# Kernel tuning notes

Hardware: AMD Instinct MI355X
Metric: run time of the kernel (lower is better)

## Reference

```python
import jax, jax.numpy as jnp
import numpy as np

EPS = 1e-5
SCALE = 4


def _conv(x, w, b=None, stride=1, pad=0):
    y = jax.lax.conv_general_dilated(
        x, w, (stride, stride), ((pad, pad), (pad, pad)),
        dimension_numbers=("NCHW", "OIHW", "NCHW"))
    if b is not None:
        y = y + b[None, :, None, None]
    return y


def _bn(x, g, b, m, v):
    # inference-mode BatchNorm2d with running stats
    scale = g / jnp.sqrt(v + EPS)
    return (x - m[None, :, None, None]) * scale[None, :, None, None] + b[None, :, None, None]


def setup_inputs() -> dict:
    key = jax.random.key(0)
    ks = jax.random.split(key, 20)
    B, H, W = 2, 112, 256
    d = {}
    d["patch"] = jax.random.normal(ks[0], (B, 3, SCALE * H, SCALE * W), jnp.float32)
    d["disp"] = jax.random.normal(ks[1], (B, 1, H, W), jnp.float32)
    # encode: conv(3->256, k=s=4, no bias) + BN + ReLU + conv(256->256, k3 p1, no bias) + BN + ReLU
    d["w_enc1"] = jax.random.normal(ks[2], (256, 3, SCALE, SCALE), jnp.float32) * 0.05
    d["bn1_g"] = jax.random.uniform(ks[3], (256,), jnp.float32) + 0.5
    d["bn1_b"] = jax.random.normal(ks[4], (256,), jnp.float32) * 0.01
    d["bn1_m"] = jax.random.normal(ks[5], (256,), jnp.float32) * 0.01
    d["bn1_v"] = jax.random.uniform(ks[6], (256,), jnp.float32) + 0.5
    d["w_enc2"] = jax.random.normal(ks[7], (256, 256, 3, 3), jnp.float32) * 0.02
    d["bn2_g"] = jax.random.uniform(ks[8], (256,), jnp.float32) + 0.5
    d["bn2_b"] = jax.random.normal(ks[9], (256,), jnp.float32) * 0.01
    d["bn2_m"] = jax.random.normal(ks[10], (256,), jnp.float32) * 0.01
    d["bn2_v"] = jax.random.uniform(ks[11], (256,), jnp.float32) + 0.5
    # conv_disp_feat: conv(257->256, k3 p1) + ReLU + conv(256->512, k3 p1) + ReLU + conv(512->144, k1)
    d["w_c1"] = jax.random.normal(ks[12], (256, 257, 3, 3), jnp.float32) * 0.02
    d["b_c1"] = jax.random.normal(ks[13], (256,), jnp.float32) * 0.01
    d["w_c2"] = jax.random.normal(ks[14], (512, 256, 3, 3), jnp.float32) * 0.02
    d["b_c2"] = jax.random.normal(ks[15], (512,), jnp.float32) * 0.01
    d["w_c3"] = jax.random.normal(ks[16], (SCALE * SCALE * 9, 512, 1, 1), jnp.float32) * 0.02
    d["b_c3"] = jax.random.normal(ks[17], (SCALE * SCALE * 9,), jnp.float32) * 0.01
    return d


def reference(patch, disp, w_enc1, bn1_g, bn1_b, bn1_m, bn1_v,
              w_enc2, bn2_g, bn2_b, bn2_m, bn2_v,
              w_c1, b_c1, w_c2, b_c2, w_c3, b_c3):
    B, _, H, W = disp.shape
    # encoder
    feat = jax.nn.relu(_bn(_conv(patch, w_enc1, stride=SCALE), bn1_g, bn1_b, bn1_m, bn1_v))
    feat = jax.nn.relu(_bn(_conv(feat, w_enc2, pad=1), bn2_g, bn2_b, bn2_m, bn2_v))
    # mask prediction
    x = jnp.concatenate([disp, feat], axis=1)  # (B, 257, H, W)
    x = jax.nn.relu(_conv(x, w_c1, b_c1, pad=1))
    x = jax.nn.relu(_conv(x, w_c2, b_c2, pad=1))
    raw_mask = _conv(x, w_c3, b_c3)  # (B, 144, H, W)
    mask = raw_mask.reshape(B, 1, 9, SCALE, SCALE, H, W)
    mask = jax.nn.softmax(mask, axis=2)
    # F.unfold(disp, k=3, p=1): gather 3x3 neighborhoods, order (ky, kx)
    padd = jnp.pad(disp, ((0, 0), (0, 0), (1, 1), (1, 1)))
    neigh = jnp.stack([padd[:, :, ky:ky + H, kx:kx + W]
                       for ky in range(3) for kx in range(3)], axis=2)  # (B,1,9,H,W)
    up = (mask * neigh[:, :, :, None, None, :, :]).sum(axis=2)  # (B,1,s,s,H,W)
    up = up.transpose(0, 1, 4, 2, 5, 3).reshape(B, 1, SCALE * H, SCALE * W)
    return up
```

## Files before the change

### kernel.cpp

```cpp
#include <hip/hip_runtime.h>
#include <hip/hip_bf16.h>

constexpr int B_ = 2;
constexpr int H_ = 112;
constexpr int W_ = 256;
constexpr int HW_ = H_ * W_;
constexpr int PH_ = 448;
constexpr int PW_ = 1024;
constexpr float EPS_ = 1e-5f;

typedef __bf16 bf16x8 __attribute__((ext_vector_type(8)));
typedef float f32x4 __attribute__((ext_vector_type(4)));

__device__ __forceinline__ bf16x8 ld_bf16x8(const __hip_bfloat16* p) {
    return *reinterpret_cast<const bf16x8*>(p);
}
__device__ __forceinline__ bf16x8 zero_bf16x8() {
    union { int4 i; bf16x8 v; } u;
    u.i = make_int4(0, 0, 0, 0);
    return u.v;
}
__device__ __forceinline__ void gload_lds16(const __hip_bfloat16* g, __hip_bfloat16* lds) {
    __builtin_amdgcn_global_load_lds(
        (const __attribute__((address_space(1))) void*)g,
        (__attribute__((address_space(3))) void*)lds, 16, 0, 0);
}

__global__ void prep_w3_pack(const float* __restrict__ w, int COUT, int CSRC, int COFF,
                             const float* __restrict__ g, const float* __restrict__ vvar,
                             __hip_bfloat16* __restrict__ dst) {
    int idx = blockIdx.x * 256 + threadIdx.x;
    int CF = COUT / 16;
    int n = 9 * 8 * CF * 512;
    if (idx >= n) return;
    int j = idx & 7;
    int lane = (idx >> 3) & 63;
    int rest = idx >> 9;
    int cf = rest % CF;
    int rest2 = rest / CF;
    int ks = rest2 & 7;
    int tap = rest2 >> 3;
    int cout = cf * 16 + (lane & 15);
    int ci = ks * 32 + (lane >> 4) * 8 + j;
    float sc = g ? g[cout] * rsqrtf(vvar[cout] + EPS_) : 1.f;
    dst[idx] = __float2bfloat16(w[((size_t)cout * CSRC + ci + COFF) * 9 + tap] * sc);
}

__global__ void prep_c3_pack(const float* __restrict__ w, __hip_bfloat16* __restrict__ dst) {
    int idx = blockIdx.x * 256 + threadIdx.x;
    if (idx >= 16 * 9 * 512) return;
    int j = idx & 7;
    int lane = (idx >> 3) & 63;
    int rest = idx >> 9;
    int mf = rest % 9;
    int ks = rest / 9;
    int row = mf * 16 + (lane & 15);
    int ci = ks * 32 + (lane >> 4) * 8 + j;
    dst[idx] = __float2bfloat16(w[(size_t)row * 512 + ci]);
}

__global__ void prep_misc_kernel(const float* __restrict__ w_c1,
                                 const float* __restrict__ g, const float* __restrict__ bb,
                                 const float* __restrict__ m, const float* __restrict__ v,
                                 float* __restrict__ wd_c1, float* __restrict__ bias2) {
    int idx = blockIdx.x * 256 + threadIdx.x;
    if (idx < 256 * 9) {
        int co = idx / 9, tap = idx % 9;
        wd_c1[idx] = w_c1[(size_t)co * 257 * 9 + tap];
    } else if (idx < 256 * 9 + 256) {
        int co = idx - 256 * 9;
        float sc = g[co] * rsqrtf(v[co] + EPS_);
        bias2[co] = bb[co] - m[co] * sc;
    }
}

__global__ __launch_bounds__(256) void enc1_nhwc_kernel(
    const float* __restrict__ patch, const float* __restrict__ wgt,
    const float* __restrict__ g, const float* __restrict__ bb,
    const float* __restrict__ m, const float* __restrict__ v,
    __hip_bfloat16* __restrict__ out) {
    const int tid = threadIdx.x;
    const int px = tid & 63;
    const int wid = tid >> 6;
    const int bx = blockIdx.x;
    const int w0 = (bx & 3) * 64;
    const int h = bx >> 2;
    const int b = blockIdx.z;
    const int w = w0 + px;

    float p[3][4][4];
#pragma unroll
    for (int c = 0; c < 3; ++c)
#pragma unroll
        for (int ky = 0; ky < 4; ++ky) {
            float4 f = *reinterpret_cast<const float4*>(
                patch + (((size_t)b * 3 + c) * PH_ + 4 * h + ky) * PW_ + 4 * w);
            p[c][ky][0] = f.x; p[c][ky][1] = f.y; p[c][ky][2] = f.z; p[c][ky][3] = f.w;
        }

    __shared__ __hip_bfloat16 s[64][258];

    const int kbase = __builtin_amdgcn_readfirstlane(wid * 64);
    for (int i = 0; i < 64; ++i) {
        int k = kbase + i;
        const float* wk = wgt + (size_t)k * 48;
        float acc = 0.f;
#pragma unroll
        for (int c = 0; c < 3; ++c)
#pragma unroll
            for (int ky = 0; ky < 4; ++ky)
#pragma unroll
                for (int kx = 0; kx < 4; ++kx)
                    acc += p[c][ky][kx] * wk[(c * 4 + ky) * 4 + kx];
        float sc = g[k] * rsqrtf(v[k] + EPS_);
        float o = fmaxf(acc * sc + (bb[k] - m[k] * sc), 0.f);
        s[px][k] = __float2bfloat16(o);
    }
    __syncthreads();
    const size_t base = (((size_t)b * H_ + h) * W_ + w0) * 256;
    for (int j = tid; j < 64 * 128; j += 256) {
        int elem = j * 2;
        int pp = elem >> 8;
        int k = elem & 255;
        unsigned int val = *reinterpret_cast<const unsigned int*>(&s[pp][k]);
        *reinterpret_cast<unsigned int*>(out + base + elem) = val;
    }
}

template <int COUT, bool HAS_DISP>
__global__ __launch_bounds__(512, 4) void conv3x3_mfma5(
    const __hip_bfloat16* __restrict__ in,
    const __hip_bfloat16* __restrict__ wPack,
    const float* __restrict__ bias,
    const float* __restrict__ disp,
    const float* __restrict__ wd,
    __hip_bfloat16* __restrict__ out) {
    constexpr int CIN = 256;
    constexpr int CF = COUT / 16;
    const int tid = threadIdx.x;
    const int lane = tid & 63;
    const int wid = tid >> 6;
    const int wm = wid & 3;
    const int wn = wid >> 2;
    const int lr = lane & 15;
    const int lg = lane >> 4;

    const int bx = blockIdx.x;
    const int w0 = (bx & 1) * 128;
    const int h = bx >> 1;
    const int coutBase = blockIdx.y * 256;
    const int b = blockIdx.z;

    const int coutW = coutBase + wm * 64;
    const int cfW = coutW >> 4;
    const int pxW = wn * 64;

    __shared__ __hip_bfloat16 sIn[2][3][130][32];

    f32x4 acc[4][4] = {};

    const __hip_bfloat16* inb = in + (size_t)b * HW_ * CIN;
    const __hip_bfloat16* wBase = wPack + (size_t)cfW * 512 + (size_t)lane * 8;

    auto STAGE = [&](int buf, int c0) {
#pragma unroll
        for (int i = 0; i < 3; ++i) {
            const int idx = wid * 3 + i;
            const int row = idx >> 3, grp = idx & 7;
            const int y = h + row - 1;
            __hip_bfloat16* ldsb = &sIn[buf][row][1 + grp * 16][0];
            if ((unsigned)y < (unsigned)H_) {
                const __hip_bfloat16* gp = inb +
                    ((size_t)y * W_ + w0 + grp * 16 + (lane >> 2)) * CIN + c0 + (lane & 3) * 8;
                gload_lds16(gp, ldsb);
            } else {
                *reinterpret_cast<int4*>(reinterpret_cast<char*>(ldsb) + lane * 16) =
                    make_int4(0, 0, 0, 0);
            }
        }
        if (tid < 24) {
            const int row = tid >> 3, p2 = (tid >> 2) & 1, sub = tid & 3;
            const int pxl = p2 ? 129 : 0;
            const int y = h + row - 1, x = w0 + pxl - 1;
            bf16x8 v = zero_bf16x8();
            if ((unsigned)y < (unsigned)H_ && (unsigned)x < (unsigned)W_)
                v = ld_bf16x8(inb + ((size_t)y * W_ + x) * CIN + c0 + sub * 8);
            *reinterpret_cast<bf16x8*>(&sIn[buf][row][pxl][sub * 8]) = v;
        }
    };

    STAGE(0, 0);
    __syncthreads();
    int cur = 0;
    for (int ks = 0; ks < 8; ++ks) {
        if (ks < 7) STAGE(cur ^ 1, (ks + 1) * 32);
#pragma unroll
        for (int tap = 0; tap < 9; ++tap) {
            const int ky = tap / 3, kx = tap % 3;
            bf16x8 a[4];
#pragma unroll
            for (int mf = 0; mf < 4; ++mf)
                a[mf] = ld_bf16x8(wBase + ((size_t)(tap * 8 + ks) * CF + mf) * 512);
            bf16x8 bv[4];
#pragma unroll
            for (int nf = 0; nf < 4; ++nf)
                bv[nf] = *reinterpret_cast<const bf16x8*>(
                    &sIn[cur][ky][pxW + nf * 16 + lr + kx][lg * 8]);
            __builtin_amdgcn_s_setprio(1);
#pragma unroll
            for (int nf = 0; nf < 4; ++nf)
#pragma unroll
                for (int mf = 0; mf < 4; ++mf)
                    acc[mf][nf] = __builtin_amdgcn_mfma_f32_16x16x32_bf16(
                        a[mf], bv[nf], acc[mf][nf], 0, 0, 0);
            __builtin_amdgcn_s_setprio(0);
        }
        __syncthreads();
        cur ^= 1;
    }

    const size_t rowBase = ((size_t)b * H_ + h) * W_;
#pragma unroll
    for (int nf = 0; nf < 4; ++nf) {
        const int px = w0 + pxW + nf * 16 + lr;
        float dnb[9];
        if (HAS_DISP) {
#pragma unroll
            for (int t = 0; t < 9; ++t) {
                int yy = h + t / 3 - 1, xx = px + t % 3 - 1;
                dnb[t] = ((unsigned)yy < (unsigned)H_ && (unsigned)xx < (unsigned)W_)
                             ? disp[((size_t)b * H_ + yy) * W_ + xx]
                             : 0.f;
            }
        }
#pragma unroll
        for (int mf = 0; mf < 4; ++mf) {
            alignas(8) __hip_bfloat16 ov[4];
#pragma unroll
            for (int r = 0; r < 4; ++r) {
                const int cout = coutW + mf * 16 + lg * 4 + r;
                float o = acc[mf][nf][r] + bias[cout];
                if (HAS_DISP) {
                    float s = 0.f;
#pragma unroll
                    for (int t = 0; t < 9; ++t) s += wd[cout * 9 + t] * dnb[t];
                    o += s;
                }
                ov[r] = __float2bfloat16(fmaxf(o, 0.f));
            }
            *reinterpret_cast<uint2*>(out + (rowBase + px) * COUT + coutW + mf * 16 + lg * 4) =
                *reinterpret_cast<const uint2*>(ov);
        }
    }
}

__global__ __launch_bounds__(256) void c3_fused_kernel(
    const __hip_bfloat16* __restrict__ x2,
    const __hip_bfloat16* __restrict__ wPack,
    const float* __restrict__ bias,
    const float* __restrict__ disp,
    float* __restrict__ outp) {
    const int tid = threadIdx.x;
    const int lane = tid & 63;
    const int wid = tid >> 6;
    const int lr = lane & 15;
    const int lg = lane >> 4;
    const int bx = blockIdx.x;
    const int w0 = (bx & 3) * 64;
    const int h = bx >> 2;
    const int b = blockIdx.z;
    const int pxw = w0 + wid * 16 + lr;

    f32x4 acc[9] = {};
    const __hip_bfloat16* inp = x2 + (((size_t)b * H_ + h) * W_ + pxw) * 512;
    const __hip_bfloat16* wl = wPack + (size_t)lane * 8;
#pragma unroll 4
    for (int ks = 0; ks < 16; ++ks) {
        const int c0 = ks * 32 + lg * 8;
        bf16x8 bv = ld_bf16x8(inp + c0);
#pragma unroll
        for (int mf = 0; mf < 9; ++mf) {
            bf16x8 av = ld_bf16x8(wl + ((size_t)ks * 9 + mf) * 512);
            acc[mf] = __builtin_amdgcn_mfma_f32_16x16x32_bf16(av, bv, acc[mf], 0, 0, 0);
        }
    }

    float dnb[9];
#pragma unroll
    for (int t = 0; t < 9; ++t) {
        int yy = h + t / 3 - 1, xx = pxw + t % 3 - 1;
        dnb[t] = ((unsigned)yy < (unsigned)H_ && (unsigned)xx < (unsigned)W_)
                     ? disp[((size_t)b * H_ + yy) * W_ + xx]
                     : 0.f;
    }
    float oo[4];
#pragma unroll
    for (int r = 0; r < 4; ++r) {
        const int st = lg * 4 + r;
        float sv[9], mx = -1e30f;
#pragma unroll
        for (int mf = 0; mf < 9; ++mf) {
            sv[mf] = acc[mf][r] + bias[mf * 16 + st];
            mx = fmaxf(mx, sv[mf]);
        }
        float sum = 0.f, wsum = 0.f;
#pragma unroll
        for (int mf = 0; mf < 9; ++mf) {
            float e = __expf(sv[mf] - mx);
            sum += e;
            wsum += e * dnb[mf];
        }
        oo[r] = wsum / sum;
    }
    float4 o4 = make_float4(oo[0], oo[1], oo[2], oo[3]);
    *reinterpret_cast<float4*>(outp + ((size_t)b * PH_ + 4 * h + lg) * PW_ + 4 * pxw) = o4;
}

extern "C" void kernel_launch(void* const* d_in, const int* in_sizes, int n_in,
                              void* d_out, int out_size, void* d_ws, size_t ws_size,
                              hipStream_t stream) {
    const float* patch = (const float*)d_in[0];
    const float* disp = (const float*)d_in[1];
    const float* w_enc1 = (const float*)d_in[2];
    const float* bn1_g = (const float*)d_in[3];
    const float* bn1_b = (const float*)d_in[4];
    const float* bn1_m = (const float*)d_in[5];
    const float* bn1_v = (const float*)d_in[6];
    const float* w_enc2 = (const float*)d_in[7];
    const float* bn2_g = (const float*)d_in[8];
    const float* bn2_b = (const float*)d_in[9];
    const float* bn2_m = (const float*)d_in[10];
    const float* bn2_v = (const float*)d_in[11];
    const float* w_c1 = (const float*)d_in[12];
    const float* b_c1 = (const float*)d_in[13];
    const float* w_c2 = (const float*)d_in[14];
    const float* b_c2 = (const float*)d_in[15];
    const float* w_c3 = (const float*)d_in[16];
    const float* b_c3 = (const float*)d_in[17];
    float* out = (float*)d_out;

    char* ws = (char*)d_ws;
    const size_t S1 = (size_t)B_ * HW_ * 256 * sizeof(__hip_bfloat16);
    const size_t S2 = (size_t)B_ * HW_ * 512 * sizeof(__hip_bfloat16);
    __hip_bfloat16* feat1 = (__hip_bfloat16*)ws;   ws += S1;
    __hip_bfloat16* feat2 = (__hip_bfloat16*)ws;   ws += S1;
    __hip_bfloat16* x1    = (__hip_bfloat16*)ws;   ws += S1;
    __hip_bfloat16* x2    = (__hip_bfloat16*)ws;   ws += S2;
    __hip_bfloat16* wP_enc2 = (__hip_bfloat16*)ws; ws += (size_t)9 * 256 * 256 * 2;
    __hip_bfloat16* wP_c1   = (__hip_bfloat16*)ws; ws += (size_t)9 * 256 * 256 * 2;
    __hip_bfloat16* wP_c2   = (__hip_bfloat16*)ws; ws += (size_t)9 * 512 * 256 * 2;
    __hip_bfloat16* wP_c3   = (__hip_bfloat16*)ws; ws += (size_t)16 * 9 * 512 * 2;
    float* bias2 = (float*)ws;                     ws += 256 * 4;
    float* wd_c1 = (float*)ws;                     ws += 256 * 9 * 4;

    dim3 blk(256, 1, 1);
    dim3 blk2(512, 1, 1);

    prep_w3_pack<<<dim3((9 * 256 * 256 + 255) / 256), blk, 0, stream>>>(
        w_enc2, 256, 256, 0, bn2_g, bn2_v, wP_enc2);
    prep_w3_pack<<<dim3((9 * 256 * 256 + 255) / 256), blk, 0, stream>>>(
        w_c1, 256, 257, 1, nullptr, nullptr, wP_c1);
    prep_w3_pack<<<dim3((9 * 512 * 256 + 255) / 256), blk, 0, stream>>>(
        w_c2, 512, 256, 0, nullptr, nullptr, wP_c2);
    prep_c3_pack<<<dim3((16 * 9 * 512 + 255) / 256), blk, 0, stream>>>(w_c3, wP_c3);
    prep_misc_kernel<<<dim3((256 * 9 + 256 + 255) / 256), blk, 0, stream>>>(
        w_c1, bn2_g, bn2_b, bn2_m, bn2_v, wd_c1, bias2);

    enc1_nhwc_kernel<<<dim3(H_ * 4, 1, B_), blk, 0, stream>>>(
        patch, w_enc1, bn1_g, bn1_b, bn1_m, bn1_v, feat1);
    conv3x3_mfma5<256, false><<<dim3(2 * H_, 1, B_), blk2, 0, stream>>>(
        feat1, wP_enc2, bias2, nullptr, nullptr, feat2);
    conv3x3_mfma5<256, true><<<dim3(2 * H_, 1, B_), blk2, 0, stream>>>(
        feat2, wP_c1, b_c1, disp, wd_c1, x1);
    conv3x3_mfma5<512, false><<<dim3(2 * H_, 2, B_), blk2, 0, stream>>>(
        x1, wP_c2, b_c2, nullptr, nullptr, x2);
    c3_fused_kernel<<<dim3(H_ * 4, 1, B_), blk, 0, stream>>>(
        x2, wP_c3, b_c3, disp, out);
}
```

Baseline: 375.8 us.

## Use dedicated producer wave for LDS staging in 3x3 conv kernels

Restructures the 3x3 conv MFMA kernel into a producer/consumer layout. One extra wave does all the global-to-LDS staging, and four compute waves do the MFMAs. The output-channel tile per block is halved to 128, so the grid doubles along y. This is meant to take load issue off the compute waves so they can keep MFMAs going, at the cost of one idle-ish wave per block, more blocks that each restage the same input rows, and the removal of the occupancy hint in launch_bounds.

```diff
diff --git a/kernel.cpp b/kernel.cpp
--- a/kernel.cpp
+++ b/kernel.cpp
@@ -128,7 +128,7 @@
 }
 
 template <int COUT, bool HAS_DISP>
-__global__ __launch_bounds__(512, 4) void conv3x3_mfma5(
+__global__ __launch_bounds__(320) void conv3x3_pc(
     const __hip_bfloat16* __restrict__ in,
     const __hip_bfloat16* __restrict__ wPack,
     const float* __restrict__ bias,
@@ -140,20 +140,20 @@
     const int tid = threadIdx.x;
     const int lane = tid & 63;
     const int wid = tid >> 6;
-    const int wm = wid & 3;
-    const int wn = wid >> 2;
     const int lr = lane & 15;
     const int lg = lane >> 4;
 
     const int bx = blockIdx.x;
     const int w0 = (bx & 1) * 128;
     const int h = bx >> 1;
-    const int coutBase = blockIdx.y * 256;
+    const int coutBase = blockIdx.y * 128;
     const int b = blockIdx.z;
 
+    const int wm = wid & 1;
+    const int wn = wid >> 1;
     const int coutW = coutBase + wm * 64;
     const int cfW = coutW >> 4;
-    const int pxW = wn * 64;
+    const int pxW = (wn & 1) * 64;
 
     __shared__ __hip_bfloat16 sIn[2][3][130][32];
 
@@ -164,9 +164,8 @@
 
     auto STAGE = [&](int buf, int c0) {
 #pragma unroll
-        for (int i = 0; i < 3; ++i) {
-            const int idx = wid * 3 + i;
-            const int row = idx >> 3, grp = idx & 7;
+        for (int i = 0; i < 24; ++i) {
+            const int row = i >> 3, grp = i & 7;
             const int y = h + row - 1;
             __hip_bfloat16* ldsb = &sIn[buf][row][1 + grp * 16][0];
             if ((unsigned)y < (unsigned)H_) {
@@ -178,8 +177,8 @@
                     make_int4(0, 0, 0, 0);
             }
         }
-        if (tid < 24) {
-            const int row = tid >> 3, p2 = (tid >> 2) & 1, sub = tid & 3;
+        if (lane < 24) {
+            const int row = lane >> 3, p2 = (lane >> 2) & 1, sub = lane & 3;
             const int pxl = p2 ? 129 : 0;
             const int y = h + row - 1, x = w0 + pxl - 1;
             bf16x8 v = zero_bf16x8();
@@ -189,35 +188,40 @@
         }
     };
 
-    STAGE(0, 0);
+    if (wid == 4) STAGE(0, 0);
     __syncthreads();
-    int cur = 0;
-    for (int ks = 0; ks < 8; ++ks) {
-        if (ks < 7) STAGE(cur ^ 1, (ks + 1) * 32);
-#pragma unroll
-        for (int tap = 0; tap < 9; ++tap) {
-            const int ky = tap / 3, kx = tap % 3;
-            bf16x8 a[4];
-#pragma unroll
-            for (int mf = 0; mf < 4; ++mf)
-                a[mf] = ld_bf16x8(wBase + ((size_t)(tap * 8 + ks) * CF + mf) * 512);
-            bf16x8 bv[4];
-#pragma unroll
-            for (int nf = 0; nf < 4; ++nf)
-                bv[nf] = *reinterpret_cast<const bf16x8*>(
-                    &sIn[cur][ky][pxW + nf * 16 + lr + kx][lg * 8]);
-            __builtin_amdgcn_s_setprio(1);
-#pragma unroll
-            for (int nf = 0; nf < 4; ++nf)
+
+    for (int k = 0; k < 8; ++k) {
+        if (wid == 4) {
+            if (k < 7) STAGE((k + 1) & 1, (k + 1) * 32);
+        } else {
+            const int cur = k & 1;
+#pragma unroll
+            for (int tap = 0; tap < 9; ++tap) {
+                const int ky = tap / 3, kx = tap % 3;
+                bf16x8 a[4];
 #pragma unroll
                 for (int mf = 0; mf < 4; ++mf)
-                    acc[mf][nf] = __builtin_amdgcn_mfma_f32_16x16x32_bf16(
-                        a[mf], bv[nf], acc[mf][nf], 0, 0, 0);
-            __builtin_amdgcn_s_setprio(0);
+                    a[mf] = ld_bf16x8(wBase + ((size_t)(tap * 8 + k) * CF + mf) * 512);
+                bf16x8 bv[4];
+#pragma unroll
+                for (int nf = 0; nf < 4; ++nf)
+                    bv[nf] = *reinterpret_cast<const bf16x8*>(
+                        &sIn[cur][ky][pxW + nf * 16 + lr + kx][lg * 8]);
+                __builtin_amdgcn_s_setprio(1);
+#pragma unroll
+                for (int nf = 0; nf < 4; ++nf)
+#pragma unroll
+                    for (int mf = 0; mf < 4; ++mf)
+                        acc[mf][nf] = __builtin_amdgcn_mfma_f32_16x16x32_bf16(
+                            a[mf], bv[nf], acc[mf][nf], 0, 0, 0);
+                __builtin_amdgcn_s_setprio(0);
+            }
         }
         __syncthreads();
-        cur ^= 1;
-    }
+    }
+
+    if (wid == 4) return;
 
     const size_t rowBase = ((size_t)b * H_ + h) * W_;
 #pragma unroll
@@ -354,7 +358,7 @@
     float* wd_c1 = (float*)ws;                     ws += 256 * 9 * 4;
 
     dim3 blk(256, 1, 1);
-    dim3 blk2(512, 1, 1);
+    dim3 blkPC(320, 1, 1);
 
     prep_w3_pack<<<dim3((9 * 256 * 256 + 255) / 256), blk, 0, stream>>>(
         w_enc2, 256, 256, 0, bn2_g, bn2_v, wP_enc2);
@@ -368,11 +372,11 @@
 
     enc1_nhwc_kernel<<<dim3(H_ * 4, 1, B_), blk, 0, stream>>>(
         patch, w_enc1, bn1_g, bn1_b, bn1_m, bn1_v, feat1);
-    conv3x3_mfma5<256, false><<<dim3(2 * H_, 1, B_), blk2, 0, stream>>>(
+    conv3x3_pc<256, false><<<dim3(2 * H_, 2, B_), blkPC, 0, stream>>>(
         feat1, wP_enc2, bias2, nullptr, nullptr, feat2);
-    conv3x3_mfma5<256, true><<<dim3(2 * H_, 1, B_), blk2, 0, stream>>>(
+    conv3x3_pc<256, true><<<dim3(2 * H_, 2, B_), blkPC, 0, stream>>>(
         feat2, wP_c1, b_c1, disp, wd_c1, x1);
-    conv3x3_mfma5<512, false><<<dim3(2 * H_, 2, B_), blk2, 0, stream>>>(
+    conv3x3_pc<512, false><<<dim3(2 * H_, 4, B_), blkPC, 0, stream>>>(
         x1, wP_c2, b_c2, nullptr, nullptr, x2);
     c3_fused_kernel<<<dim3(H_ * 4, 1, B_), blk, 0, stream>>>(
         x2, wP_c3, b_c3, disp, out);
```

New measurement: 542.7 us. 44.4% more time.
